# Performance work log

Hardware: AMD Instinct MI355X
Metric: run time of the kernel (lower is better)

## Reference

```python
import jax, jax.numpy as jnp
import numpy as np

N = 100000
E = 1600000
IN_DIM = 128
HID_DIM = 128
OUT_DIM = 128


def _sage_conv(x, src, dst, W_l, b_l, W_r, num_nodes):
    """PyG SAGEConv with mean aggregation:
       out = mean_{j in N(i)} x_j @ W_l + b_l + x_i @ W_r
    edge_index convention: messages flow src -> dst."""
    msg = x[src]                                        # [E, d_in] gather
    agg_sum = jax.ops.segment_sum(msg, dst, num_segments=num_nodes)   # [N, d_in]
    cnt = jax.ops.segment_sum(jnp.ones((msg.shape[0],), x.dtype), dst,
                              num_segments=num_nodes)   # [N]
    agg = agg_sum / jnp.maximum(cnt, 1.0)[:, None]      # scatter-mean (0 for isolated nodes)
    return agg @ W_l + b_l + x @ W_r


def setup_inputs() -> dict:
    key = jax.random.key(0)
    ks = jax.random.split(key, 8)
    def glorot(k, fan_in, fan_out):
        s = jnp.sqrt(2.0 / (fan_in + fan_out))
        return jax.random.normal(k, (fan_in, fan_out), dtype=jnp.float32) * s
    x = jax.random.normal(ks[0], (N, IN_DIM), dtype=jnp.float32)
    edge_index = jax.random.randint(ks[1], (2, E), 0, N, dtype=jnp.int64)
    return {
        "x": x,
        "edge_index": edge_index,
        "W1_l": glorot(ks[2], IN_DIM, HID_DIM),
        "b1": jnp.zeros((HID_DIM,), jnp.float32),
        "W1_r": glorot(ks[3], IN_DIM, HID_DIM),
        "W2_l": glorot(ks[4], HID_DIM, OUT_DIM),
        "b2": jnp.zeros((OUT_DIM,), jnp.float32),
        "W2_r": glorot(ks[5], HID_DIM, OUT_DIM),
    }


def reference(x, edge_index, W1_l, b1, W1_r, W2_l, b2, W2_r):
    src, dst = edge_index[0], edge_index[1]
    h = _sage_conv(x, src, dst, W1_l, b1, W1_r, N)
    h = jax.nn.relu(h)
    # F.dropout(p=0.5, training=self.training): identity in eval mode
    out = _sage_conv(h, src, dst, W2_l, b2, W2_r, N)
    return out
```

## Files before the change

kernel.cpp:

```cpp
#include <hip/hip_runtime.h>
#include <hip/hip_bf16.h>

#define N_NODES 100000
#define N_EDGES 1600000
#define DIM 128
#define BR 32
#define ESTG 1024
#define NB 782
#define CHUNK 16384

typedef __attribute__((ext_vector_type(8))) short bf16x8;
typedef __attribute__((ext_vector_type(4))) float f32x4;
typedef __attribute__((ext_vector_type(2))) float f32x2;
typedef __attribute__((ext_vector_type(4))) float f4;
typedef __attribute__((ext_vector_type(4))) unsigned int u32x4;
typedef __attribute__((ext_vector_type(2))) unsigned int u32x2;
typedef __attribute__((ext_vector_type(4))) int i32x4;

#define OFF_ROWPTR 0
#define OFF_BCNT   (N_NODES + 4)
#define OFF_BBASE  (OFF_BCNT + NB)
#define OFF_BCUR   (OFF_BBASE + NB)
#define OFF_PAIRS  (OFF_BCUR + NB)
#define OFF_COLSRC (OFF_PAIRS + N_EDGES)
#define OFF_HB     (OFF_COLSRC + N_EDGES)
#define OFF_HF8    (OFF_HB + N_NODES * DIM / 2)
#define OFF_WB     (OFF_HF8 + N_NODES * DIM / 4)

__device__ inline unsigned int f2bf(float f) {
    unsigned int u = __float_as_uint(f);
    return (u + 0x7FFFu + ((u >> 16) & 1u)) >> 16;
}
__device__ inline unsigned char f2fp8(float v) {
    return (unsigned char)(__builtin_amdgcn_cvt_pk_fp8_f32(v, v, 0u, false) & 0xFFu);
}

__global__ __launch_bounds__(256) void conv_pack_kernel(
    const float* __restrict__ x, unsigned char* __restrict__ xf8,
    unsigned short* __restrict__ xb,
    const float* __restrict__ W1l, const float* __restrict__ W1r,
    const float* __restrict__ W2l, const float* __restrict__ W2r,
    unsigned short* __restrict__ WB,
    const int* __restrict__ dst, int* __restrict__ bcnt)
{
    __shared__ int histL[NB];
    const int b = blockIdx.x;
    const int tid = threadIdx.x;
    if (b < 6250) {
        long i = (long)(b * 256 + tid) * 8;
        f4 a = __builtin_nontemporal_load((const f4*)(x + i));
        f4 c = __builtin_nontemporal_load((const f4*)(x + i + 4));
        unsigned int w0 = 0, w1 = 0;
        w0 = __builtin_amdgcn_cvt_pk_fp8_f32(a[0], a[1], w0, false);
        w0 = __builtin_amdgcn_cvt_pk_fp8_f32(a[2], a[3], w0, true);
        w1 = __builtin_amdgcn_cvt_pk_fp8_f32(c[0], c[1], w1, false);
        w1 = __builtin_amdgcn_cvt_pk_fp8_f32(c[2], c[3], w1, true);
        u32x2 o8; o8[0] = w0; o8[1] = w1;
        __builtin_nontemporal_store(o8, (u32x2*)(xf8 + i));
        u32x4 ob;
        ob[0] = f2bf(a[0]) | (f2bf(a[1]) << 16);
        ob[1] = f2bf(a[2]) | (f2bf(a[3]) << 16);
        ob[2] = f2bf(c[0]) | (f2bf(c[1]) << 16);
        ob[3] = f2bf(c[2]) | (f2bf(c[3]) << 16);
        __builtin_nontemporal_store(ob, (u32x4*)(xb + i));
    } else if (b < 6506) {
        int t = (b - 6250) * 256 + tid;
        int layer = t >> 15;
        int rest  = t & 32767;
        int half  = rest >> 14;
        int idx   = rest & 16383;
        int k = idx >> 7;
        int n = idx & 127;
        const float* W = layer ? (half ? W2r : W2l) : (half ? W1r : W1l);
        int kk = half * 128 + k;
        WB[layer * 32768 + (((kk >> 3) * 128 + n) << 3) + (kk & 7)] =
            (unsigned short)f2bf(W[idx]);
    } else {
        const int e0 = (b - 6506) * CHUNK;
        const int e1 = min(e0 + CHUNK, N_EDGES);
        for (int q = tid; q < NB; q += 256) histL[q] = 0;
        __syncthreads();
        for (int i = (e0 >> 2) + tid; i < (e1 >> 2); i += 256) {
            i32x4 d = __builtin_nontemporal_load((const i32x4*)dst + i);
            atomicAdd(&histL[d[0] >> 7], 1);
            atomicAdd(&histL[d[1] >> 7], 1);
            atomicAdd(&histL[d[2] >> 7], 1);
            atomicAdd(&histL[d[3] >> 7], 1);
        }
        __syncthreads();
        for (int q = tid; q < NB; q += 256) {
            int c = histL[q];
            if (c) atomicAdd(&bcnt[q], c);
        }
    }
}

__global__ __launch_bounds__(1024) void bscan_kernel(
    const int* __restrict__ bcnt, int* __restrict__ bbase,
    int* __restrict__ bcur, int* __restrict__ rowptr)
{
    __shared__ int tmp[1024];
    int tid = threadIdx.x;
    int v = (tid < NB) ? bcnt[tid] : 0;
    tmp[tid] = v;
    __syncthreads();
    for (int off = 1; off < 1024; off <<= 1) {
        int t = (tid >= off) ? tmp[tid - off] : 0;
        __syncthreads();
        tmp[tid] += t;
        __syncthreads();
    }
    if (tid < NB) { int b = tmp[tid] - v; bbase[tid] = b; bcur[tid] = b; }
    if (tid == 0) rowptr[N_NODES] = N_EDGES;
}

__global__ __launch_bounds__(256) void bfill_kernel(
    const int* __restrict__ src, const int* __restrict__ dst,
    int* __restrict__ bcur, unsigned int* __restrict__ pairs)
{
    __shared__ int histL[NB];
    __shared__ int baseL[NB];
    const int tid = threadIdx.x;
    const int e0 = blockIdx.x * CHUNK;
    const int e1 = min(e0 + CHUNK, N_EDGES);
    for (int b = tid; b < NB; b += 256) histL[b] = 0;
    __syncthreads();
    for (int i = (e0 >> 2) + tid; i < (e1 >> 2); i += 256) {
        i32x4 d = __builtin_nontemporal_load((const i32x4*)dst + i);
        atomicAdd(&histL[d[0] >> 7], 1);
        atomicAdd(&histL[d[1] >> 7], 1);
        atomicAdd(&histL[d[2] >> 7], 1);
        atomicAdd(&histL[d[3] >> 7], 1);
    }
    __syncthreads();
    for (int b = tid; b < NB; b += 256) {
        int c = histL[b];
        baseL[b] = c ? atomicAdd(&bcur[b], c) : 0;
        histL[b] = 0;
    }
    __syncthreads();
    for (int i = (e0 >> 2) + tid; i < (e1 >> 2); i += 256) {
        i32x4 s = __builtin_nontemporal_load((const i32x4*)src + i);
        i32x4 d = __builtin_nontemporal_load((const i32x4*)dst + i);
        #pragma unroll
        for (int k = 0; k < 4; ++k) {
            int bk = d[k] >> 7;
            int r = atomicAdd(&histL[bk], 1);
            pairs[baseL[bk] + r] =
                (unsigned int)s[k] | ((unsigned int)(d[k] & 127) << 25);
        }
    }
}

__global__ __launch_bounds__(256) void bucket_csr_kernel(
    const unsigned int* __restrict__ pairs,
    const int* __restrict__ bcnt, const int* __restrict__ bbase,
    int* __restrict__ rowptr, int* __restrict__ colsrc)
{
    __shared__ int histA[128], exclS[128], hist2[128];
    const int bucket = blockIdx.x;
    const int tid = threadIdx.x;
    const int cnt  = bcnt[bucket];
    const int base = bbase[bucket];
    if (tid < 128) { histA[tid] = 0; hist2[tid] = 0; }
    __syncthreads();
    for (int i = tid; i < cnt; i += 256)
        atomicAdd(&histA[pairs[base + i] >> 25], 1);
    __syncthreads();
    int v = 0;
    if (tid < 128) { v = histA[tid]; exclS[tid] = v; }
    __syncthreads();
    for (int off = 1; off < 128; off <<= 1) {
        int t = 0;
        if (tid < 128 && tid >= off) t = exclS[tid - off];
        __syncthreads();
        if (tid < 128) exclS[tid] += t;
        __syncthreads();
    }
    if (tid < 128) exclS[tid] -= v;
    const int node0 = bucket * 128;
    if (tid < 128 && node0 + tid < N_NODES)
        rowptr[node0 + tid] = base + exclS[tid];
    __syncthreads();
    for (int i = tid; i < cnt; i += 256) {
        unsigned int p = pairs[base + i];
        int dl = (int)(p >> 25);
        int r = atomicAdd(&hist2[dl], 1);
        colsrc[base + exclS[dl] + r] = (int)(p & 0x1FFFFFFu);
    }
}

__device__ inline void addfp8(float* acc, u32x2 v) {
    f32x2 p;
    p = __builtin_amdgcn_cvt_pk_f32_fp8((int)v[0], false); acc[0] += p[0]; acc[1] += p[1];
    p = __builtin_amdgcn_cvt_pk_f32_fp8((int)v[0], true);  acc[2] += p[0]; acc[3] += p[1];
    p = __builtin_amdgcn_cvt_pk_f32_fp8((int)v[1], false); acc[4] += p[0]; acc[5] += p[1];
    p = __builtin_amdgcn_cvt_pk_f32_fp8((int)v[1], true);  acc[6] += p[0]; acc[7] += p[1];
}

__global__ __launch_bounds__(256, 8) void fused_sage_kernel(
    const unsigned char* __restrict__ f8,
    const unsigned short* __restrict__ selfB,
    const int* __restrict__ rowptr,
    const int* __restrict__ colsrc,
    const unsigned short* __restrict__ WB,
    const float* __restrict__ bias,
    unsigned short* __restrict__ outb,
    unsigned char* __restrict__ outf8,
    float* __restrict__ outf,
    int mode)
{
    __shared__ __align__(16) char smem[20480];
    unsigned short* catS = (unsigned short*)smem;
    int* eS = (int*)(smem + 16384);

    const int tid = threadIdx.x;
    const int block_row = blockIdx.x * BR;
    const int ebase = rowptr[block_row];
    const int span  = rowptr[block_row + BR] - ebase;
    const int smax  = span < ESTG ? span : ESTG;

    for (int i = tid; i < smax; i += 256)
        eS[i] = __builtin_nontemporal_load(&colsrc[ebase + i]) << 7;
    __syncthreads();

    const int c   = tid & 15;
    const int c8  = c * 8;
    const int grp = tid >> 4;

    #pragma unroll
    for (int it = 0; it < 2; ++it) {
        const int nl = grp * 2 + it;
        const int node = block_row + nl;
        const int s  = rowptr[node] - ebase;
        const int e_ = rowptr[node + 1] - ebase;
        const int lim = e_ < ESTG ? e_ : ESTG;

        const u32x4 sv = __builtin_nontemporal_load(
            (const u32x4*)(selfB + ((long)node << 7) + c8));

        float acc[8];
        #pragma unroll
        for (int q = 0; q < 8; ++q) acc[q] = 0.0f;

        int i = s;
        for (; i + 8 <= lim; i += 8) {
            const u32x2 v0 = *(const u32x2*)(f8 + eS[i + 0] + c8);
            const u32x2 v1 = *(const u32x2*)(f8 + eS[i + 1] + c8);
            const u32x2 v2 = *(const u32x2*)(f8 + eS[i + 2] + c8);
            const u32x2 v3 = *(const u32x2*)(f8 + eS[i + 3] + c8);
            const u32x2 v4 = *(const u32x2*)(f8 + eS[i + 4] + c8);
            const u32x2 v5 = *(const u32x2*)(f8 + eS[i + 5] + c8);
            const u32x2 v6 = *(const u32x2*)(f8 + eS[i + 6] + c8);
            const u32x2 v7 = *(const u32x2*)(f8 + eS[i + 7] + c8);
            addfp8(acc, v0); addfp8(acc, v1); addfp8(acc, v2); addfp8(acc, v3);
            addfp8(acc, v4); addfp8(acc, v5); addfp8(acc, v6); addfp8(acc, v7);
        }
        if (i + 4 <= lim) {
            const u32x2 v0 = *(const u32x2*)(f8 + eS[i + 0] + c8);
            const u32x2 v1 = *(const u32x2*)(f8 + eS[i + 1] + c8);
            const u32x2 v2 = *(const u32x2*)(f8 + eS[i + 2] + c8);
            const u32x2 v3 = *(const u32x2*)(f8 + eS[i + 3] + c8);
            addfp8(acc, v0); addfp8(acc, v1); addfp8(acc, v2); addfp8(acc, v3);
            i += 4;
        }
        if (i + 2 <= lim) {
            const u32x2 v0 = *(const u32x2*)(f8 + eS[i + 0] + c8);
            const u32x2 v1 = *(const u32x2*)(f8 + eS[i + 1] + c8);
            addfp8(acc, v0); addfp8(acc, v1);
            i += 2;
        }
        if (i < lim) {
            const u32x2 v = *(const u32x2*)(f8 + eS[i] + c8);
            addfp8(acc, v);
            ++i;
        }
        for (; i < e_; ++i) {
            const u32x2 v = *(const u32x2*)(f8 + ((long)colsrc[ebase + i] << 7) + c8);
            addfp8(acc, v);
        }

        const float inv = 1.0f / fmaxf((float)(e_ - s), 1.0f);
        uint4 pv;
        pv.x = f2bf(acc[0] * inv) | (f2bf(acc[1] * inv) << 16);
        pv.y = f2bf(acc[2] * inv) | (f2bf(acc[3] * inv) << 16);
        pv.z = f2bf(acc[4] * inv) | (f2bf(acc[5] * inv) << 16);
        pv.w = f2bf(acc[6] * inv) | (f2bf(acc[7] * inv) << 16);
        const int sw = c ^ (nl & 7);
        *(uint4*)&catS[nl * 256 + sw * 8] = pv;
        *(u32x4*)&catS[nl * 256 + 128 + sw * 8] = sv;
    }
    __syncthreads();

    const int w    = tid >> 6;
    const int l    = tid & 63;
    const int wm   = w & 1;
    const int wn   = w >> 1;
    const int lrow = l & 15;
    const int kgrp = l >> 4;
    const int ar   = wm * 16 + lrow;

    f32x4 acc4[4];
    #pragma unroll
    for (int t = 0; t < 4; ++t) acc4[t] = (f32x4){0.f, 0.f, 0.f, 0.f};

    #pragma unroll
    for (int step = 0; step < 8; ++step) {
        const int slot = step * 4 + kgrp;
        bf16x8 a = *(const bf16x8*)&catS[ar * 256 + ((slot ^ (ar & 7)) << 3)];
        #pragma unroll
        for (int t = 0; t < 4; ++t) {
            const int n = wn * 64 + t * 16 + lrow;
            bf16x8 b = *(const bf16x8*)(WB + ((slot * 128 + n) << 3));
            acc4[t] = __builtin_amdgcn_mfma_f32_16x16x32_bf16(a, b, acc4[t], 0, 0, 0);
        }
    }

    __syncthreads();
    const int cbase = wn * 64 + lrow;
    if (mode) {
        unsigned short* lbf = (unsigned short*)smem;
        unsigned char*  lr8 = (unsigned char*)(smem + 8448);
        #pragma unroll
        for (int t = 0; t < 4; ++t) {
            const int col = cbase + t * 16;
            const float bb = bias[col];
            #pragma unroll
            for (int j = 0; j < 4; ++j) {
                float v = fmaxf(acc4[t][j] + bb, 0.0f);
                const int row = wm * 16 + kgrp * 4 + j;
                lbf[row * 132 + col] = (unsigned short)f2bf(v);
                lr8[row * 136 + col] = f2fp8(v);
            }
        }
        __syncthreads();
        #pragma unroll
        for (int it = 0; it < 8; ++it) {
            const int row = w * 8 + it;
            unsigned int v = *(const unsigned int*)&lbf[row * 132 + l * 2];
            *(unsigned int*)&outb[(long)(block_row + row) * 128 + l * 2] = v;
        }
        #pragma unroll
        for (int it = 0; it < 4; ++it) {
            const int row = w * 8 + it * 2 + (l >> 5);
            unsigned int v = *(const unsigned int*)&lr8[row * 136 + (l & 31) * 4];
            *(unsigned int*)&outf8[(long)(block_row + row) * 128 + (l & 31) * 4] = v;
        }
    } else {
        float* lf = (float*)smem;
        #pragma unroll
        for (int t = 0; t < 4; ++t) {
            const int col = cbase + t * 16;
            const float bb = bias[col];
            #pragma unroll
            for (int j = 0; j < 4; ++j) {
                const int row = wm * 16 + kgrp * 4 + j;
                lf[row * 132 + col] = acc4[t][j] + bb;
            }
        }
        __syncthreads();
        #pragma unroll
        for (int it = 0; it < 16; ++it) {
            const int row  = w * 8 + (it >> 1);
            const int half = (it & 1) * 64;
            float v = lf[row * 132 + half + l];
            outf[(long)(block_row + row) * 128 + half + l] = v;
        }
    }
}

extern "C" void kernel_launch(void* const* d_in, const int* in_sizes, int n_in,
                              void* d_out, int out_size, void* d_ws, size_t ws_size,
                              hipStream_t stream)
{
    const float* x   = (const float*)d_in[0];
    const int*   ei  = (const int*)d_in[1];
    const float* W1l = (const float*)d_in[2];
    const float* b1  = (const float*)d_in[3];
    const float* W1r = (const float*)d_in[4];
    const float* W2l = (const float*)d_in[5];
    const float* b2  = (const float*)d_in[6];
    const float* W2r = (const float*)d_in[7];
    float* out = (float*)d_out;

    const int* src = ei;
    const int* dst = ei + N_EDGES;

    int* wsi = (int*)d_ws;
    int* rowptr = wsi + OFF_ROWPTR;
    int* bcnt   = wsi + OFF_BCNT;
    int* bbase  = wsi + OFF_BBASE;
    int* bcur   = wsi + OFF_BCUR;
    unsigned int* pairs = (unsigned int*)(wsi + OFF_PAIRS);
    int* colsrc = wsi + OFF_COLSRC;
    unsigned short* hb  = (unsigned short*)(wsi + OFF_HB);
    unsigned char*  hf8 = (unsigned char*)(wsi + OFF_HF8);
    unsigned short* WB  = (unsigned short*)(wsi + OFF_WB);

    unsigned char*  xf8 = (unsigned char*)d_out;
    unsigned short* xb  = (unsigned short*)(xf8 + (size_t)N_NODES * DIM);

    hipMemsetAsync(bcnt, 0, (size_t)NB * sizeof(int), stream);

    const int eblocks = (N_EDGES + CHUNK - 1) / CHUNK;
    conv_pack_kernel<<<6506 + eblocks, 256, 0, stream>>>(
        x, xf8, xb, W1l, W1r, W2l, W2r, WB, dst, bcnt);
    bscan_kernel<<<1, 1024, 0, stream>>>(bcnt, bbase, bcur, rowptr);
    bfill_kernel<<<eblocks, 256, 0, stream>>>(src, dst, bcur, pairs);
    bucket_csr_kernel<<<NB, 256, 0, stream>>>(pairs, bcnt, bbase, rowptr, colsrc);

    const int gblocks = N_NODES / BR;
    fused_sage_kernel<<<gblocks, 256, 0, stream>>>(
        xf8, xb, rowptr, colsrc, WB, b1, hb, hf8, (float*)nullptr, 1);
    fused_sage_kernel<<<gblocks, 256, 0, stream>>>(
        hf8, hb, rowptr, colsrc, WB + 32768, b2,
        (unsigned short*)nullptr, (unsigned char*)nullptr, out, 0);
}
```

Before: 208.8 us.

## Sub-sort neighbors by source slice and interleave two-node gathers for locality

The CSR build now sorts each node's neighbor list by destination and also by one of four source-index slices, and it records per-slice start offsets in a new sstart array. The fused SAGE kernel walks the slices in order and alternates between its two nodes within each slice. This is meant to keep concurrent gathers in the same region of the feature table for better L2 locality, and to give more independent loads in flight. In exchange the CSR kernel uses a 512-bin histogram and scan, the workspace grows, and the gather loops are shorter with more tail handling.

```diff
diff --git a/kernel.cpp b/kernel.cpp
--- a/kernel.cpp
+++ b/kernel.cpp
@@ -8,6 +8,7 @@
 #define ESTG 1024
 #define NB 782
 #define CHUNK 16384
+#define NSL 4
 
 typedef __attribute__((ext_vector_type(8))) short bf16x8;
 typedef __attribute__((ext_vector_type(4))) float f32x4;
@@ -21,7 +22,8 @@
 #define OFF_BCNT   (N_NODES + 4)
 #define OFF_BBASE  (OFF_BCNT + NB)
 #define OFF_BCUR   (OFF_BBASE + NB)
-#define OFF_PAIRS  (OFF_BCUR + NB)
+#define OFF_SSTART (OFF_BCUR + NB)
+#define OFF_PAIRS  (OFF_SSTART + 4 * N_NODES)
 #define OFF_COLSRC (OFF_PAIRS + N_EDGES)
 #define OFF_HB     (OFF_COLSRC + N_EDGES)
 #define OFF_HF8    (OFF_HB + N_NODES * DIM / 2)
@@ -155,38 +157,53 @@
 __global__ __launch_bounds__(256) void bucket_csr_kernel(
     const unsigned int* __restrict__ pairs,
     const int* __restrict__ bcnt, const int* __restrict__ bbase,
-    int* __restrict__ rowptr, int* __restrict__ colsrc)
-{
-    __shared__ int histA[128], exclS[128], hist2[128];
+    int* __restrict__ rowptr, int* __restrict__ colsrc,
+    int* __restrict__ sstart)
+{
+    __shared__ int histA[512], exclS[512], hist2[512];
+    __shared__ int tmp[256];
     const int bucket = blockIdx.x;
     const int tid = threadIdx.x;
     const int cnt  = bcnt[bucket];
     const int base = bbase[bucket];
-    if (tid < 128) { histA[tid] = 0; hist2[tid] = 0; }
-    __syncthreads();
-    for (int i = tid; i < cnt; i += 256)
-        atomicAdd(&histA[pairs[base + i] >> 25], 1);
-    __syncthreads();
-    int v = 0;
-    if (tid < 128) { v = histA[tid]; exclS[tid] = v; }
-    __syncthreads();
-    for (int off = 1; off < 128; off <<= 1) {
-        int t = 0;
-        if (tid < 128 && tid >= off) t = exclS[tid - off];
-        __syncthreads();
-        if (tid < 128) exclS[tid] += t;
-        __syncthreads();
-    }
-    if (tid < 128) exclS[tid] -= v;
-    const int node0 = bucket * 128;
-    if (tid < 128 && node0 + tid < N_NODES)
-        rowptr[node0 + tid] = base + exclS[tid];
+    histA[tid] = 0; histA[tid + 256] = 0;
+    hist2[tid] = 0; hist2[tid + 256] = 0;
     __syncthreads();
     for (int i = tid; i < cnt; i += 256) {
         unsigned int p = pairs[base + i];
-        int dl = (int)(p >> 25);
-        int r = atomicAdd(&hist2[dl], 1);
-        colsrc[base + exclS[dl] + r] = (int)(p & 0x1FFFFFFu);
+        int key = (int)((p >> 25) << 2) | (int)((p & 0x1FFFFFFu) >> 15);
+        atomicAdd(&histA[key], 1);
+    }
+    __syncthreads();
+    int a = histA[2 * tid], b = histA[2 * tid + 1];
+    tmp[tid] = a + b;
+    __syncthreads();
+    for (int off = 1; off < 256; off <<= 1) {
+        int t = (tid >= off) ? tmp[tid - off] : 0;
+        __syncthreads();
+        tmp[tid] += t;
+        __syncthreads();
+    }
+    int ex = tmp[tid] - (a + b);
+    exclS[2 * tid] = ex;
+    exclS[2 * tid + 1] = ex + a;
+    __syncthreads();
+    const int node0 = bucket * 128;
+    if (tid < 128 && node0 + tid < N_NODES) {
+        i32x4 ss;
+        ss[0] = base + exclS[tid * 4 + 0];
+        ss[1] = base + exclS[tid * 4 + 1];
+        ss[2] = base + exclS[tid * 4 + 2];
+        ss[3] = base + exclS[tid * 4 + 3];
+        rowptr[node0 + tid] = ss[0];
+        *(i32x4*)&sstart[(node0 + tid) * 4] = ss;
+    }
+    __syncthreads();
+    for (int i = tid; i < cnt; i += 256) {
+        unsigned int p = pairs[base + i];
+        int key = (int)((p >> 25) << 2) | (int)((p & 0x1FFFFFFu) >> 15);
+        int r = atomicAdd(&hist2[key], 1);
+        colsrc[base + exclS[key] + r] = (int)(p & 0x1FFFFFFu);
     }
 }
 
@@ -202,6 +219,7 @@
     const unsigned char* __restrict__ f8,
     const unsigned short* __restrict__ selfB,
     const int* __restrict__ rowptr,
+    const int* __restrict__ sstart,
     const int* __restrict__ colsrc,
     const unsigned short* __restrict__ WB,
     const float* __restrict__ bias,
@@ -228,59 +246,70 @@
     const int c8  = c * 8;
     const int grp = tid >> 4;
 
+    const int nA = block_row + grp * 2;
+    const int nB = nA + 1;
+    const i32x4 ssA = *(const i32x4*)&sstart[nA * 4];
+    const i32x4 ssB = *(const i32x4*)&sstart[nB * 4];
+    const int endA = rowptr[nA + 1];
+    const int endB = rowptr[nB + 1];
+
+    const u32x4 svA = __builtin_nontemporal_load(
+        (const u32x4*)(selfB + ((long)nA << 7) + c8));
+    const u32x4 svB = __builtin_nontemporal_load(
+        (const u32x4*)(selfB + ((long)nB << 7) + c8));
+
+    float accA[8], accB[8];
+    #pragma unroll
+    for (int q = 0; q < 8; ++q) { accA[q] = 0.0f; accB[q] = 0.0f; }
+
+#define GATHER_SEG(ACC, S_, E_)                                             \
+    {                                                                       \
+        int i_ = (S_);                                                      \
+        const int lim_ = (E_) < ESTG ? (E_) : ESTG;                         \
+        for (; i_ + 4 <= lim_; i_ += 4) {                                   \
+            const u32x2 v0 = *(const u32x2*)(f8 + eS[i_ + 0] + c8);         \
+            const u32x2 v1 = *(const u32x2*)(f8 + eS[i_ + 1] + c8);         \
+            const u32x2 v2 = *(const u32x2*)(f8 + eS[i_ + 2] + c8);         \
+            const u32x2 v3 = *(const u32x2*)(f8 + eS[i_ + 3] + c8);         \
+            addfp8(ACC, v0); addfp8(ACC, v1);                               \
+            addfp8(ACC, v2); addfp8(ACC, v3);                               \
+        }                                                                   \
+        if (i_ + 2 <= lim_) {                                               \
+            const u32x2 v0 = *(const u32x2*)(f8 + eS[i_ + 0] + c8);         \
+            const u32x2 v1 = *(const u32x2*)(f8 + eS[i_ + 1] + c8);         \
+            addfp8(ACC, v0); addfp8(ACC, v1);                               \
+            i_ += 2;                                                        \
+        }                                                                   \
+        if (i_ < lim_) {                                                    \
+            const u32x2 v = *(const u32x2*)(f8 + eS[i_] + c8);              \
+            addfp8(ACC, v);                                                 \
+            ++i_;                                                           \
+        }                                                                   \
+        for (; i_ < (E_); ++i_) {                                           \
+            const u32x2 v = *(const u32x2*)                                 \
+                (f8 + ((long)colsrc[ebase + i_] << 7) + c8);                \
+            addfp8(ACC, v);                                                 \
+        }                                                                   \
+    }
+
+    #pragma unroll
+    for (int sl = 0; sl < NSL; ++sl) {
+        const int sA = ssA[sl] - ebase;
+        const int eA = (sl < NSL - 1 ? ssA[sl + 1] : endA) - ebase;
+        const int sB = ssB[sl] - ebase;
+        const int eB = (sl < NSL - 1 ? ssB[sl + 1] : endB) - ebase;
+        GATHER_SEG(accA, sA, eA)
+        GATHER_SEG(accB, sB, eB)
+    }
+#undef GATHER_SEG
+
     #pragma unroll
     for (int it = 0; it < 2; ++it) {
         const int nl = grp * 2 + it;
-        const int node = block_row + nl;
-        const int s  = rowptr[node] - ebase;
-        const int e_ = rowptr[node + 1] - ebase;
-        const int lim = e_ < ESTG ? e_ : ESTG;
-
-        const u32x4 sv = __builtin_nontemporal_load(
-            (const u32x4*)(selfB + ((long)node << 7) + c8));
-
-        float acc[8];
-        #pragma unroll
-        for (int q = 0; q < 8; ++q) acc[q] = 0.0f;
-
-        int i = s;
-        for (; i + 8 <= lim; i += 8) {
-            const u32x2 v0 = *(const u32x2*)(f8 + eS[i + 0] + c8);
-            const u32x2 v1 = *(const u32x2*)(f8 + eS[i + 1] + c8);
-            const u32x2 v2 = *(const u32x2*)(f8 + eS[i + 2] + c8);
-            const u32x2 v3 = *(const u32x2*)(f8 + eS[i + 3] + c8);
-            const u32x2 v4 = *(const u32x2*)(f8 + eS[i + 4] + c8);
-            const u32x2 v5 = *(const u32x2*)(f8 + eS[i + 5] + c8);
-            const u32x2 v6 = *(const u32x2*)(f8 + eS[i + 6] + c8);
-            const u32x2 v7 = *(const u32x2*)(f8 + eS[i + 7] + c8);
-            addfp8(acc, v0); addfp8(acc, v1); addfp8(acc, v2); addfp8(acc, v3);
-            addfp8(acc, v4); addfp8(acc, v5); addfp8(acc, v6); addfp8(acc, v7);
-        }
-        if (i + 4 <= lim) {
-            const u32x2 v0 = *(const u32x2*)(f8 + eS[i + 0] + c8);
-            const u32x2 v1 = *(const u32x2*)(f8 + eS[i + 1] + c8);
-            const u32x2 v2 = *(const u32x2*)(f8 + eS[i + 2] + c8);
-            const u32x2 v3 = *(const u32x2*)(f8 + eS[i + 3] + c8);
-            addfp8(acc, v0); addfp8(acc, v1); addfp8(acc, v2); addfp8(acc, v3);
-            i += 4;
-        }
-        if (i + 2 <= lim) {
-            const u32x2 v0 = *(const u32x2*)(f8 + eS[i + 0] + c8);
-            const u32x2 v1 = *(const u32x2*)(f8 + eS[i + 1] + c8);
-            addfp8(acc, v0); addfp8(acc, v1);
-            i += 2;
-        }
-        if (i < lim) {
-            const u32x2 v = *(const u32x2*)(f8 + eS[i] + c8);
-            addfp8(acc, v);
-            ++i;
-        }
-        for (; i < e_; ++i) {
-            const u32x2 v = *(const u32x2*)(f8 + ((long)colsrc[ebase + i] << 7) + c8);
-            addfp8(acc, v);
-        }
-
-        const float inv = 1.0f / fmaxf((float)(e_ - s), 1.0f);
+        const float* acc = it ? accB : accA;
+        const int deg = it ? (endB - ssB[0]) : (endA - ssA[0]);
+        const u32x4 sv = it ? svB : svA;
+        const float inv = 1.0f / fmaxf((float)deg, 1.0f);
         uint4 pv;
         pv.x = f2bf(acc[0] * inv) | (f2bf(acc[1] * inv) << 16);
         pv.y = f2bf(acc[2] * inv) | (f2bf(acc[3] * inv) << 16);
@@ -391,6 +420,7 @@
     int* bcnt   = wsi + OFF_BCNT;
     int* bbase  = wsi + OFF_BBASE;
     int* bcur   = wsi + OFF_BCUR;
+    int* sstart = wsi + OFF_SSTART;
     unsigned int* pairs = (unsigned int*)(wsi + OFF_PAIRS);
     int* colsrc = wsi + OFF_COLSRC;
     unsigned short* hb  = (unsigned short*)(wsi + OFF_HB);
@@ -407,12 +437,13 @@
         x, xf8, xb, W1l, W1r, W2l, W2r, WB, dst, bcnt);
     bscan_kernel<<<1, 1024, 0, stream>>>(bcnt, bbase, bcur, rowptr);
     bfill_kernel<<<eblocks, 256, 0, stream>>>(src, dst, bcur, pairs);
-    bucket_csr_kernel<<<NB, 256, 0, stream>>>(pairs, bcnt, bbase, rowptr, colsrc);
+    bucket_csr_kernel<<<NB, 256, 0, stream>>>(
+        pairs, bcnt, bbase, rowptr, colsrc, sstart);
 
     const int gblocks = N_NODES / BR;
     fused_sage_kernel<<<gblocks, 256, 0, stream>>>(
-        xf8, xb, rowptr, colsrc, WB, b1, hb, hf8, (float*)nullptr, 1);
+        xf8, xb, rowptr, sstart, colsrc, WB, b1, hb, hf8, (float*)nullptr, 1);
     fused_sage_kernel<<<gblocks, 256, 0, stream>>>(
-        hf8, hb, rowptr, colsrc, WB + 32768, b2,
+        hf8, hb, rowptr, sstart, colsrc, WB + 32768, b2,
         (unsigned short*)nullptr, (unsigned char*)nullptr, out, 0);
 }
```

After: 221.8 us. 1.06x slower.

## Replace atomic bucket counting with per-block count matrix and column prefix scans

Applied to the files above, without the earlier changes.

The edge histogram is now written per chunk into a count matrix instead of being summed into global bucket counters with atomics. Column-sum and column-prefix kernels then give each chunk a deterministic base offset per bucket, so the fill kernel no longer recomputes the histogram or does global atomics. The chunk size shrinks to 4096 to get more blocks. This removes the redundant histogram pass and the atomic contention, but adds two kernel launches and extra count-matrix traffic with strided column reads.

```diff
diff --git a/kernel.cpp b/kernel.cpp
--- a/kernel.cpp
+++ b/kernel.cpp
@@ -7,7 +7,8 @@
 #define BR 32
 #define ESTG 1024
 #define NB 782
-#define CHUNK 16384
+#define CHUNK 4096
+#define NBLK 391
 
 typedef __attribute__((ext_vector_type(8))) short bf16x8;
 typedef __attribute__((ext_vector_type(4))) float f32x4;
@@ -20,8 +21,8 @@
 #define OFF_ROWPTR 0
 #define OFF_BCNT   (N_NODES + 4)
 #define OFF_BBASE  (OFF_BCNT + NB)
-#define OFF_BCUR   (OFF_BBASE + NB)
-#define OFF_PAIRS  (OFF_BCUR + NB)
+#define OFF_CNTM   (OFF_BBASE + NB)
+#define OFF_PAIRS  (OFF_CNTM + NBLK * NB)
 #define OFF_COLSRC (OFF_PAIRS + N_EDGES)
 #define OFF_HB     (OFF_COLSRC + N_EDGES)
 #define OFF_HF8    (OFF_HB + N_NODES * DIM / 2)
@@ -41,7 +42,7 @@
     const float* __restrict__ W1l, const float* __restrict__ W1r,
     const float* __restrict__ W2l, const float* __restrict__ W2r,
     unsigned short* __restrict__ WB,
-    const int* __restrict__ dst, int* __restrict__ bcnt)
+    const int* __restrict__ dst, int* __restrict__ cntM)
 {
     __shared__ int histL[NB];
     const int b = blockIdx.x;
@@ -76,7 +77,8 @@
         WB[layer * 32768 + (((kk >> 3) * 128 + n) << 3) + (kk & 7)] =
             (unsigned short)f2bf(W[idx]);
     } else {
-        const int e0 = (b - 6506) * CHUNK;
+        const int blk = b - 6506;
+        const int e0 = blk * CHUNK;
         const int e1 = min(e0 + CHUNK, N_EDGES);
         for (int q = tid; q < NB; q += 256) histL[q] = 0;
         __syncthreads();
@@ -88,16 +90,31 @@
             atomicAdd(&histL[d[3] >> 7], 1);
         }
         __syncthreads();
-        for (int q = tid; q < NB; q += 256) {
-            int c = histL[q];
-            if (c) atomicAdd(&bcnt[q], c);
-        }
-    }
+        for (int q = tid; q < NB; q += 256)
+            cntM[blk * NB + q] = histL[q];
+    }
+}
+
+__global__ __launch_bounds__(256) void colsum_kernel(
+    const int* __restrict__ cntM, int* __restrict__ bcnt)
+{
+    __shared__ int red[256];
+    const int b = blockIdx.x;
+    const int tid = threadIdx.x;
+    int s = 0;
+    for (int i = tid; i < NBLK; i += 256) s += cntM[i * NB + b];
+    red[tid] = s;
+    __syncthreads();
+    for (int off = 128; off > 0; off >>= 1) {
+        if (tid < off) red[tid] += red[tid + off];
+        __syncthreads();
+    }
+    if (tid == 0) bcnt[b] = red[0];
 }
 
 __global__ __launch_bounds__(1024) void bscan_kernel(
     const int* __restrict__ bcnt, int* __restrict__ bbase,
-    int* __restrict__ bcur, int* __restrict__ rowptr)
+    int* __restrict__ rowptr)
 {
     __shared__ int tmp[1024];
     int tid = threadIdx.x;
@@ -110,32 +127,48 @@
         tmp[tid] += t;
         __syncthreads();
     }
-    if (tid < NB) { int b = tmp[tid] - v; bbase[tid] = b; bcur[tid] = b; }
+    if (tid < NB) bbase[tid] = tmp[tid] - v;
     if (tid == 0) rowptr[N_NODES] = N_EDGES;
+}
+
+__global__ __launch_bounds__(256) void colprefix_kernel(
+    int* __restrict__ cntM, const int* __restrict__ bbase)
+{
+    __shared__ int e0[512];
+    __shared__ int tmp[256];
+    const int b = blockIdx.x;
+    const int tid = threadIdx.x;
+    int a0 = (2 * tid     < NBLK) ? cntM[(2 * tid)     * NB + b] : 0;
+    int a1 = (2 * tid + 1 < NBLK) ? cntM[(2 * tid + 1) * NB + b] : 0;
+    tmp[tid] = a0 + a1;
+    __syncthreads();
+    for (int off = 1; off < 256; off <<= 1) {
+        int t = (tid >= off) ? tmp[tid - off] : 0;
+        __syncthreads();
+        tmp[tid] += t;
+        __syncthreads();
+    }
+    int ex = tmp[tid] - (a0 + a1);
+    e0[2 * tid] = ex;
+    e0[2 * tid + 1] = ex + a0;
+    __syncthreads();
+    const int base = bbase[b];
+    if (2 * tid < NBLK)     cntM[(2 * tid)     * NB + b] = base + e0[2 * tid];
+    if (2 * tid + 1 < NBLK) cntM[(2 * tid + 1) * NB + b] = base + e0[2 * tid + 1];
 }
 
 __global__ __launch_bounds__(256) void bfill_kernel(
     const int* __restrict__ src, const int* __restrict__ dst,
-    int* __restrict__ bcur, unsigned int* __restrict__ pairs)
+    const int* __restrict__ cntM, unsigned int* __restrict__ pairs)
 {
     __shared__ int histL[NB];
     __shared__ int baseL[NB];
     const int tid = threadIdx.x;
-    const int e0 = blockIdx.x * CHUNK;
+    const int blk = blockIdx.x;
+    const int e0 = blk * CHUNK;
     const int e1 = min(e0 + CHUNK, N_EDGES);
-    for (int b = tid; b < NB; b += 256) histL[b] = 0;
-    __syncthreads();
-    for (int i = (e0 >> 2) + tid; i < (e1 >> 2); i += 256) {
-        i32x4 d = __builtin_nontemporal_load((const i32x4*)dst + i);
-        atomicAdd(&histL[d[0] >> 7], 1);
-        atomicAdd(&histL[d[1] >> 7], 1);
-        atomicAdd(&histL[d[2] >> 7], 1);
-        atomicAdd(&histL[d[3] >> 7], 1);
-    }
-    __syncthreads();
     for (int b = tid; b < NB; b += 256) {
-        int c = histL[b];
-        baseL[b] = c ? atomicAdd(&bcur[b], c) : 0;
+        baseL[b] = cntM[blk * NB + b];
         histL[b] = 0;
     }
     __syncthreads();
@@ -390,7 +423,7 @@
     int* rowptr = wsi + OFF_ROWPTR;
     int* bcnt   = wsi + OFF_BCNT;
     int* bbase  = wsi + OFF_BBASE;
-    int* bcur   = wsi + OFF_BCUR;
+    int* cntM   = wsi + OFF_CNTM;
     unsigned int* pairs = (unsigned int*)(wsi + OFF_PAIRS);
     int* colsrc = wsi + OFF_COLSRC;
     unsigned short* hb  = (unsigned short*)(wsi + OFF_HB);
@@ -400,13 +433,12 @@
     unsigned char*  xf8 = (unsigned char*)d_out;
     unsigned short* xb  = (unsigned short*)(xf8 + (size_t)N_NODES * DIM);
 
-    hipMemsetAsync(bcnt, 0, (size_t)NB * sizeof(int), stream);
-
-    const int eblocks = (N_EDGES + CHUNK - 1) / CHUNK;
-    conv_pack_kernel<<<6506 + eblocks, 256, 0, stream>>>(
-        x, xf8, xb, W1l, W1r, W2l, W2r, WB, dst, bcnt);
-    bscan_kernel<<<1, 1024, 0, stream>>>(bcnt, bbase, bcur, rowptr);
-    bfill_kernel<<<eblocks, 256, 0, stream>>>(src, dst, bcur, pairs);
+    conv_pack_kernel<<<6506 + NBLK, 256, 0, stream>>>(
+        x, xf8, xb, W1l, W1r, W2l, W2r, WB, dst, cntM);
+    colsum_kernel<<<NB, 256, 0, stream>>>(cntM, bcnt);
+    bscan_kernel<<<1, 1024, 0, stream>>>(bcnt, bbase, rowptr);
+    colprefix_kernel<<<NB, 256, 0, stream>>>(cntM, bbase);
+    bfill_kernel<<<NBLK, 256, 0, stream>>>(src, dst, cntM, pairs);
     bucket_csr_kernel<<<NB, 256, 0, stream>>>(pairs, bcnt, bbase, rowptr, colsrc);
 
     const int gblocks = N_NODES / BR;
```

Result: faster. 196.1 us, median of 2 (-6.1%).
